# Kernel optimization log

Measured on AMD Instinct MI355X. Metric: run time of the kernel, lower is better.

The kernel has to match this reference:

```python
import jax, jax.numpy as jnp
import numpy as np

N_ATOMS = 100000
N_BONDS = 200000
N_MOLS = 4000
ATOMS_PER_MOL = 25
MAX_NB = 6
ATOM_FDIM = 133
BOND_FDIM = 14
HIDDEN = 300
DEPTH = 3


def setup_inputs() -> dict:
    key = jax.random.key(0)
    ks = jax.random.split(key, 8)
    f_atoms = jax.random.normal(ks[0], (N_ATOMS, ATOM_FDIM), dtype=jnp.float32)
    f_bonds = jax.random.normal(ks[1], (N_BONDS, BOND_FDIM), dtype=jnp.float32)
    # incoming-bond lists per atom (irregular gather targets)
    a2b = jax.random.randint(ks[2], (N_ATOMS, MAX_NB), 0, N_BONDS, dtype=jnp.int32)
    # source atom of each directed bond
    b2a = jax.random.randint(ks[3], (N_BONDS,), 0, N_ATOMS, dtype=jnp.int32)
    # reverse bond: directed bonds come in pairs (2i, 2i+1)
    b2revb = (jnp.arange(N_BONDS, dtype=jnp.int32) ^ 1)
    # contiguous [start, size] per molecule
    starts = jnp.arange(N_MOLS, dtype=jnp.int32) * ATOMS_PER_MOL
    sizes = jnp.full((N_MOLS,), ATOMS_PER_MOL, dtype=jnp.int32)
    a_scope = jnp.stack([starts, sizes], axis=1)
    W_i = jax.random.normal(ks[4], (HIDDEN, ATOM_FDIM + BOND_FDIM), dtype=jnp.float32) * 0.05
    W_h = jax.random.normal(ks[5], (HIDDEN, HIDDEN), dtype=jnp.float32) * 0.05
    W_o = jax.random.normal(ks[6], (HIDDEN, ATOM_FDIM + HIDDEN), dtype=jnp.float32) * 0.05
    b_o = jax.random.normal(ks[7], (HIDDEN,), dtype=jnp.float32) * 0.05
    return {"f_atoms": f_atoms, "f_bonds": f_bonds, "a2b": a2b, "b2a": b2a,
            "b2revb": b2revb, "a_scope": a_scope, "W_i": W_i, "W_h": W_h,
            "W_o": W_o, "b_o": b_o}


def reference(f_atoms, f_bonds, a2b, b2a, b2revb, a_scope, W_i, W_h, W_o, b_o):
    # initial directed-bond messages: [f_atoms[src], f_bonds] -> Linear -> ReLU
    input_feats = jnp.concatenate([f_atoms[b2a], f_bonds], axis=1)  # (E, 147)
    message = jax.nn.relu(input_feats @ W_i.T)  # (E, H)
    for _ in range(DEPTH - 1):
        nei_a_message = message[a2b].sum(axis=1)          # (V, H) gather+sum
        nei_message = nei_a_message[b2a] - message[b2revb]  # (E, H)
        message = jax.nn.relu(nei_message @ W_h.T)
    a_message = message[a2b].sum(axis=1)  # (V, H)
    atom_hiddens = jax.nn.relu(jnp.concatenate([f_atoms, a_message], axis=1) @ W_o.T + b_o)
    # vectorized scope mean-pool (scopes are contiguous ranges)
    starts = a_scope[:, 0]
    sizes = a_scope[:, 1]
    seg_ids = jnp.searchsorted(starts, jnp.arange(atom_hiddens.shape[0]), side='right') - 1
    sums = jax.ops.segment_sum(atom_hiddens, seg_ids, num_segments=N_MOLS)
    denom = jnp.maximum(sizes, 1).astype(atom_hiddens.dtype)[:, None]
    mol_vecs = jnp.where((sizes > 0)[:, None], sums / denom, 0.0)
    return mol_vecs
```

## Files before the change

### kernel.cpp

```cpp
#include <hip/hip_runtime.h>
#include <stdint.h>

#define N_ATOMS   100000
#define N_BONDS   200000
#define N_MOLS    4000
#define MAX_NB    6
#define ATOM_FDIM 133
#define BOND_FDIM 14
#define HIDDEN    300
#define NPAD      320

typedef __attribute__((ext_vector_type(8))) short          bf16x8;
typedef __attribute__((ext_vector_type(8))) unsigned short u16x8;
typedef __attribute__((ext_vector_type(4))) float          f32x4;
typedef __attribute__((ext_vector_type(4))) unsigned int   u32x4;

static __device__ __forceinline__ float u2f(unsigned int u) {
  union { unsigned int u; float f; } v; v.u = u; return v.f;
}
static __device__ __forceinline__ unsigned int f2u(float f) {
  union { float f; unsigned int u; } v; v.f = f; return v.u;
}
static __device__ __forceinline__ float bflo(unsigned int u) { return u2f(u << 16); }
static __device__ __forceinline__ float bfhi(unsigned int u) { return u2f(u & 0xffff0000u); }
static __device__ __forceinline__ unsigned short f2bf_rn(float f) {
  unsigned int u = f2u(f);
  return (unsigned short)((u + 0x7fffu + ((u >> 16) & 1u)) >> 16);
}
static __device__ __forceinline__ unsigned int pack_rn(float lo, float hi) {
  return ((unsigned int)f2bf_rn(hi) << 16) | f2bf_rn(lo);
}

__global__ __launch_bounds__(256) void convin_kernel(
    const float* __restrict__ w, unsigned short* __restrict__ o, int N, int K, int KP) {
  size_t total = (size_t)N * KP;
  for (size_t idx = (size_t)blockIdx.x * 256 + threadIdx.x; idx < total; idx += (size_t)gridDim.x * 256) {
    int n = (int)(idx / KP), k = (int)(idx - (size_t)n * KP);
    float v = (k < K) ? w[(size_t)n * K + k] : 0.f;
    o[idx] = f2bf_rn(v);
  }
}

__global__ __launch_bounds__(256) void convw_kernel(
    const float* __restrict__ w, unsigned short* __restrict__ o,
    int Ksrc, int seg1, int src2off, int seg2dst, int seg2len, int KP) {
  int total = NPAD * KP;
  for (int idx = blockIdx.x * 256 + threadIdx.x; idx < total; idx += gridDim.x * 256) {
    int n = idx / KP, k = idx - n * KP;
    int src = -1;
    if (k < seg1) src = k;
    else if (k >= seg2dst && k < seg2dst + seg2len) src = src2off + (k - seg2dst);
    float v = (n < HIDDEN && src >= 0) ? w[(size_t)n * Ksrc + src] : 0.f;
    o[idx] = f2bf_rn(v);
  }
}

template<int KP, int SEG, bool RELU, bool BIAS>
__global__ __launch_bounds__(256) void gemm_tp(
    const unsigned short* S1, const unsigned short* S2,
    const int* __restrict__ gmap, const unsigned short* __restrict__ W,
    const float* __restrict__ bias, unsigned short* out, int M, int nTiles) {
  constexpr int CHUNKS = KP / 8;
  constexpr int NST    = KP / 32;
  __shared__ __align__(16) unsigned short As[2 * 64 * KP];

  const int tid  = threadIdx.x;
  const int lane = tid & 63;
  const int wv   = tid >> 6;
  const int ar   = lane & 15, kq = lane >> 4;
  const int nbase = wv * 80;
  const unsigned short* Wl = W + (size_t)(nbase + ar) * KP + kq * 8;

  auto rowof = [&](int tile) { int r = tile * 64 + lane; return (r < M) ? r : (M - 1); };

  auto stage = [&](int buf, int drow, int srow) {
    char* base = (char*)As + (size_t)buf * (64 * KP * 2);
#pragma unroll
    for (int cs = wv; cs < CHUNKS; cs += 4) {
      const unsigned short* src;
      if (SEG == 0)      src = S1 + (size_t)drow * KP + cs * 8;
      else if (SEG == 1) src = (cs < 20) ? (S1 + (size_t)srow * 160 + cs * 8)
                                         : (S2 + (size_t)drow * 32 + (cs - 20) * 8);
      else               src = (cs < 20) ? (S1 + (size_t)drow * 160 + cs * 8)
                                         : (S2 + (size_t)drow * NPAD + (cs - 20) * 8);
      __builtin_amdgcn_global_load_lds(
          (const __attribute__((address_space(1))) void*)src,
          (__attribute__((address_space(3))) void*)(base + (size_t)cs * 1024), 16, 0, 0);
    }
  };

  f32x4 acc[4][5];

  auto compute = [&](int buf) {
    const char* base = (const char*)As + (size_t)buf * (64 * KP * 2);
    bf16x8 bnxt[5];
#pragma unroll
    for (int nf = 0; nf < 5; nf++) bnxt[nf] = *(const bf16x8*)(Wl + (size_t)nf * 16 * KP);
#pragma unroll
    for (int ks = 0; ks < NST; ks++) {
      bf16x8 bcur[5];
#pragma unroll
      for (int nf = 0; nf < 5; nf++) bcur[nf] = bnxt[nf];
      if (ks + 1 < NST) {
#pragma unroll
        for (int nf = 0; nf < 5; nf++)
          bnxt[nf] = *(const bf16x8*)(Wl + (size_t)nf * 16 * KP + (ks + 1) * 32);
      }
      bf16x8 af[4];
#pragma unroll
      for (int m = 0; m < 4; m++)
        af[m] = *(const bf16x8*)(base + (size_t)((ks * 4 + kq) * 64 + m * 16 + ar) * 16);
#pragma unroll
      for (int nf = 0; nf < 5; nf++)
#pragma unroll
        for (int m = 0; m < 4; m++)
          acc[m][nf] = __builtin_amdgcn_mfma_f32_16x16x32_bf16(af[m], bcur[nf], acc[m][nf], 0, 0, 0);
    }
  };

  auto storeC = [&](int tile) {
#pragma unroll
    for (int m = 0; m < 4; m++)
#pragma unroll
      for (int rr = 0; rr < 4; rr++) {
        int orow = tile * 64 + m * 16 + kq * 4 + rr;
        if (orow >= M) continue;
#pragma unroll
        for (int nf = 0; nf < 5; nf++) {
          int ocol = nbase + nf * 16 + ar;
          float v = acc[m][nf][rr];
          if (BIAS) v += (ocol < HIDDEN) ? bias[ocol] : 0.f;
          if (RELU) v = v > 0.f ? v : 0.f;
          out[(size_t)orow * NPAD + ocol] = f2bf_rn(v);
        }
      }
  };

  int t = blockIdx.x;
  if (t >= nTiles) return;
  {
    int srow0 = (SEG == 1) ? gmap[rowof(t)] : 0;
    stage(0, rowof(t), srow0);
  }
  int tn = t + gridDim.x;
  int g_n = (SEG == 1 && tn < nTiles) ? gmap[rowof(tn)] : 0;
  __syncthreads();

  int cur = 0;
  while (t < nTiles) {
    const int nxt = t + gridDim.x;
    if (nxt < nTiles) stage(cur ^ 1, rowof(nxt), g_n);
    const int t2 = nxt + gridDim.x;
    int g_n2 = (SEG == 1 && t2 < nTiles) ? gmap[rowof(t2)] : 0;
#pragma unroll
    for (int m = 0; m < 4; m++)
#pragma unroll
      for (int n = 0; n < 5; n++) acc[m][n] = (f32x4){0.f, 0.f, 0.f, 0.f};
    compute(cur);
    __syncthreads();
    storeC(t);
    cur ^= 1; t = nxt; g_n = g_n2;
  }
}

__global__ __launch_bounds__(256) void gemm_tpf(
    const unsigned short* Z, const unsigned short* __restrict__ Nei,
    const int* __restrict__ b2a, const unsigned short* __restrict__ W,
    unsigned short* out, int nTiles) {
  constexpr int KP = 320, NST = 10, NREG = 10;
  __shared__ __align__(16) unsigned short As[2 * 64 * KP];

  const int tid  = threadIdx.x;
  const int lane = tid & 63;
  const int wv   = tid >> 6;
  const int ar   = lane & 15, kq = lane >> 4;
  const int nbase = wv * 80;
  const unsigned short* Wl = W + (size_t)(nbase + ar) * KP + kq * 8;

  u32x4 nei4[NREG], z4[NREG];

  auto loadreg = [&](int tile) {
    const int row = tile * 64 + lane;
    const int g   = b2a[row];
    const int rev = row ^ 1;
#pragma unroll
    for (int i = 0; i < NREG; i++) {
      const int cs = i * 4 + wv;
      nei4[i] = *(const u32x4*)(Nei + (size_t)g * NPAD + cs * 8);
      z4[i]   = *(const u32x4*)(Z + (size_t)rev * NPAD + cs * 8);
    }
  };

  auto writestage = [&](int buf) {
    char* base = (char*)As + (size_t)buf * (64 * KP * 2);
#pragma unroll
    for (int i = 0; i < NREG; i++) {
      const int cs = i * 4 + wv;
      u32x4 o;
#pragma unroll
      for (int t4 = 0; t4 < 4; t4++) {
        float lo = bflo(nei4[i][t4]) - bflo(z4[i][t4]);
        float hi = bfhi(nei4[i][t4]) - bfhi(z4[i][t4]);
        lo = lo > 0.f ? lo : 0.f; hi = hi > 0.f ? hi : 0.f;
        o[t4] = pack_rn(lo, hi);
      }
      *(u32x4*)(base + (size_t)(cs * 64 + lane) * 16) = o;
    }
  };

  f32x4 acc[4][5];

  auto compute = [&](int buf) {
    const char* base = (const char*)As + (size_t)buf * (64 * KP * 2);
    bf16x8 bnxt[5];
#pragma unroll
    for (int nf = 0; nf < 5; nf++) bnxt[nf] = *(const bf16x8*)(Wl + (size_t)nf * 16 * KP);
#pragma unroll
    for (int ks = 0; ks < NST; ks++) {
      bf16x8 bcur[5];
#pragma unroll
      for (int nf = 0; nf < 5; nf++) bcur[nf] = bnxt[nf];
      if (ks + 1 < NST) {
#pragma unroll
        for (int nf = 0; nf < 5; nf++)
          bnxt[nf] = *(const bf16x8*)(Wl + (size_t)nf * 16 * KP + (ks + 1) * 32);
      }
      bf16x8 af[4];
#pragma unroll
      for (int m = 0; m < 4; m++)
        af[m] = *(const bf16x8*)(base + (size_t)((ks * 4 + kq) * 64 + m * 16 + ar) * 16);
#pragma unroll
      for (int nf = 0; nf < 5; nf++)
#pragma unroll
        for (int m = 0; m < 4; m++)
          acc[m][nf] = __builtin_amdgcn_mfma_f32_16x16x32_bf16(af[m], bcur[nf], acc[m][nf], 0, 0, 0);
    }
  };

  auto storeC = [&](int tile) {
#pragma unroll
    for (int m = 0; m < 4; m++)
#pragma unroll
      for (int rr = 0; rr < 4; rr++) {
        int orow = tile * 64 + m * 16 + kq * 4 + rr;
#pragma unroll
        for (int nf = 0; nf < 5; nf++)
          out[(size_t)orow * NPAD + nbase + nf * 16 + ar] =
              f2bf_rn(acc[m][nf][rr]);
      }
  };

  int t = blockIdx.x;
  if (t >= nTiles) return;
  loadreg(t);
  writestage(0);
  __syncthreads();

  int cur = 0;
  while (t < nTiles) {
    const int nxt = t + gridDim.x;
    if (nxt < nTiles) loadreg(nxt);
#pragma unroll
    for (int m = 0; m < 4; m++)
#pragma unroll
      for (int n = 0; n < 5; n++) acc[m][n] = (f32x4){0.f, 0.f, 0.f, 0.f};
    compute(cur);
    if (nxt < nTiles) writestage(cur ^ 1);
    __syncthreads();
    storeC(t);
    cur ^= 1; t = nxt;
  }
}

__global__ __launch_bounds__(256) void agg_kernel(
    const unsigned short* __restrict__ src, const int* __restrict__ a2b,
    unsigned short* __restrict__ dst) {
  const int TPA = NPAD / 16;
  int idx = blockIdx.x * 256 + threadIdx.x;
  if (idx >= N_ATOMS * TPA) return;
  int a  = idx / TPA;
  int kc = (idx - a * TPA) * 16;
  int bidx[MAX_NB];
#pragma unroll
  for (int j = 0; j < MAX_NB; j++) bidx[j] = a2b[a * MAX_NB + j];
  float slo[8], shi[8];
#pragma unroll
  for (int t = 0; t < 8; t++) { slo[t] = 0.f; shi[t] = 0.f; }
#pragma unroll
  for (int j = 0; j < MAX_NB; j++) {
    const u32x4* p = (const u32x4*)(src + (size_t)bidx[j] * NPAD + kc);
    u32x4 v0 = p[0], v1 = p[1];
#pragma unroll
    for (int t = 0; t < 4; t++) {
      slo[t]     += bflo(v0[t]); shi[t]     += bfhi(v0[t]);
      slo[4 + t] += bflo(v1[t]); shi[4 + t] += bfhi(v1[t]);
    }
  }
  u32x4 o0, o1;
#pragma unroll
  for (int t = 0; t < 4; t++) { o0[t] = pack_rn(slo[t], shi[t]); o1[t] = pack_rn(slo[4 + t], shi[4 + t]); }
  u32x4* qp = (u32x4*)(dst + (size_t)a * NPAD + kc);
  qp[0] = o0; qp[1] = o1;
}

__global__ __launch_bounds__(256) void combineH_kernel(
    const unsigned short* __restrict__ neiZ, const unsigned short* Zh,
    const int* __restrict__ b2a, unsigned short* msg) {
  const int TPB = NPAD / 16;
  const int NPAIR = N_BONDS / 2;
  int idx = blockIdx.x * 256 + threadIdx.x;
  if (idx >= NPAIR * TPB) return;
  int p  = idx / TPB;
  int kc = (idx - p * TPB) * 16;
  int b0i = 2 * p, b1i = 2 * p + 1;
  int g0 = b2a[b0i], g1 = b2a[b1i];
  const u32x4* pn0 = (const u32x4*)(neiZ + (size_t)g0 * NPAD + kc);
  const u32x4* pn1 = (const u32x4*)(neiZ + (size_t)g1 * NPAD + kc);
  const u32x4* pz0 = (const u32x4*)(Zh + (size_t)b1i * NPAD + kc);
  const u32x4* pz1 = (const u32x4*)(Zh + (size_t)b0i * NPAD + kc);
  u32x4 n00 = pn0[0], n01 = pn0[1], n10 = pn1[0], n11 = pn1[1];
  u32x4 z00 = pz0[0], z01 = pz0[1], z10 = pz1[0], z11 = pz1[1];
  u32x4 o00, o01, o10, o11;
#pragma unroll
  for (int t = 0; t < 4; t++) {
    float a, c;
    a = bflo(n00[t]) - bflo(z00[t]); c = bfhi(n00[t]) - bfhi(z00[t]);
    o00[t] = pack_rn(a > 0.f ? a : 0.f, c > 0.f ? c : 0.f);
    a = bflo(n01[t]) - bflo(z01[t]); c = bfhi(n01[t]) - bfhi(z01[t]);
    o01[t] = pack_rn(a > 0.f ? a : 0.f, c > 0.f ? c : 0.f);
    a = bflo(n10[t]) - bflo(z10[t]); c = bfhi(n10[t]) - bfhi(z10[t]);
    o10[t] = pack_rn(a > 0.f ? a : 0.f, c > 0.f ? c : 0.f);
    a = bflo(n11[t]) - bflo(z11[t]); c = bfhi(n11[t]) - bfhi(z11[t]);
    o11[t] = pack_rn(a > 0.f ? a : 0.f, c > 0.f ? c : 0.f);
  }
  u32x4* q0 = (u32x4*)(msg + (size_t)b0i * NPAD + kc);
  u32x4* q1 = (u32x4*)(msg + (size_t)b1i * NPAD + kc);
  q0[0] = o00; q0[1] = o01; q1[0] = o10; q1[1] = o11;
}

__global__ __launch_bounds__(256) void readout_kernel(
    const unsigned short* __restrict__ hidden, const int* __restrict__ a_scope,
    float* __restrict__ out) {
  const int TPM = NPAD / 8;
  int idx = blockIdx.x * 256 + threadIdx.x;
  if (idx >= N_MOLS * TPM) return;
  int m = idx / TPM;
  int c = (idx - m * TPM) * 8;
  int start = a_scope[m * 2], size = a_scope[m * 2 + 1];
  float s[8];
#pragma unroll
  for (int t = 0; t < 8; t++) s[t] = 0.f;
  for (int i = 0; i < size; i++) {
    const u32x4 v = *(const u32x4*)(hidden + (size_t)(start + i) * NPAD + c);
#pragma unroll
    for (int t = 0; t < 4; t++) { s[2 * t] += bflo(v[t]); s[2 * t + 1] += bfhi(v[t]); }
  }
  float inv = (size > 0) ? 1.f / (float)size : 0.f;
#pragma unroll
  for (int t = 0; t < 8; t++) {
    int col = c + t;
    if (col < HIDDEN) out[(size_t)m * HIDDEN + col] = s[t] * inv;
  }
}

extern "C" void kernel_launch(void* const* d_in, const int* in_sizes, int n_in,
                              void* d_out, int out_size, void* d_ws, size_t ws_size,
                              hipStream_t stream) {
  const float* f_atoms = (const float*)d_in[0];
  const float* f_bonds = (const float*)d_in[1];
  const int*   a2b     = (const int*)d_in[2];
  const int*   b2a     = (const int*)d_in[3];
  const int*   a_scope = (const int*)d_in[5];
  const float* W_i     = (const float*)d_in[6];
  const float* W_h     = (const float*)d_in[7];
  const float* W_o     = (const float*)d_in[8];
  const float* b_o     = (const float*)d_in[9];
  float* out = (float*)d_out;

  char* ws = (char*)d_ws;
  size_t off = 0;
  auto alloc = [&](size_t bytes) { size_t o = off; off += (bytes + 255) & ~(size_t)255; return o; };
  unsigned short* P     = (unsigned short*)(ws + alloc((size_t)N_BONDS * NPAD * 2));
  unsigned short* R     = (unsigned short*)(ws + alloc((size_t)N_ATOMS * NPAD * 2));
  unsigned short* fa_bf = (unsigned short*)(ws + alloc((size_t)N_ATOMS * 160 * 2));
  unsigned short* fb_bf = (unsigned short*)(ws + alloc((size_t)N_BONDS * 32 * 2));
  unsigned short* WiAB  = (unsigned short*)(ws + alloc((size_t)NPAD * 192 * 2));
  unsigned short* Wh    = (unsigned short*)(ws + alloc((size_t)NPAD * 320 * 2));
  unsigned short* Wo    = (unsigned short*)(ws + alloc((size_t)NPAD * 480 * 2));

  convin_kernel<<<2048, 256, 0, stream>>>(f_atoms, fa_bf, N_ATOMS, ATOM_FDIM, 160);
  convin_kernel<<<2048, 256, 0, stream>>>(f_bonds, fb_bf, N_BONDS, BOND_FDIM, 32);
  convw_kernel<<<(NPAD * 192 + 255) / 256, 256, 0, stream>>>(W_i, WiAB, 147, 133, 133, 160, 14, 192);
  convw_kernel<<<(NPAD * 320 + 255) / 256, 256, 0, stream>>>(W_h, Wh, 300, 300, 0, 0, 0, 320);
  convw_kernel<<<(NPAD * 480 + 255) / 256, 256, 0, stream>>>(W_o, Wo, 433, 133, 133, 160, 300, 480);

  const int nTilesB = N_BONDS / 64;
  const int nTilesA = (N_ATOMS + 63) / 64;
  const int gagg = (N_ATOMS * (NPAD / 16) + 255) / 256;
  const int gpar = ((N_BONDS / 2) * (NPAD / 16) + 255) / 256;

  gemm_tp<192, 1, true, false><<<768, 256, 0, stream>>>(
      fa_bf, fb_bf, b2a, WiAB, nullptr, P, N_BONDS, nTilesB);

  gemm_tp<320, 0, false, false><<<512, 256, 0, stream>>>(
      P, nullptr, nullptr, Wh, nullptr, P, N_BONDS, nTilesB);
  agg_kernel<<<gagg, 256, 0, stream>>>(P, a2b, R);

  gemm_tpf<<<512, 256, 0, stream>>>(P, R, b2a, Wh, P, nTilesB);

  agg_kernel<<<gagg, 256, 0, stream>>>(P, a2b, R);
  combineH_kernel<<<gpar, 256, 0, stream>>>(R, P, b2a, P);

  agg_kernel<<<gagg, 256, 0, stream>>>(P, a2b, R);
  gemm_tp<480, 3, true, true><<<256, 256, 0, stream>>>(
      fa_bf, R, nullptr, Wo, b_o, R, N_ATOMS, nTilesA);

  readout_kernel<<<(N_MOLS * (NPAD / 8) + 255) / 256, 256, 0, stream>>>(R, a_scope, out);
}
```

Measured before the change: 658.8 us.

## Split GEMM K dimension into double-buffered chunks to shrink LDS footprint

The tiled GEMM now stages each 64-row A tile in K-chunks (two for the input and hidden GEMMs, three for the output GEMM) instead of the whole K width. It double-buffers across chunks and tiles, cutting shared-memory use per block so more blocks can be resident per CU, and grid sizes are raised to match. The trade-off is more barriers per tile. The gather-map prefetch for the next tile is also dropped, so the index load now sits on the staging path.

After: 695.4 us. 5.6% more time.

```diff
diff --git a/kernel.cpp b/kernel.cpp
--- a/kernel.cpp
+++ b/kernel.cpp
@@ -55,14 +55,15 @@
   }
 }
 
-template<int KP, int SEG, bool RELU, bool BIAS>
-__global__ __launch_bounds__(256) void gemm_tp(
+template<int KP, int NCH, int SEG, bool RELU, bool BIAS>
+__global__ __launch_bounds__(256) void gemm_tpc(
     const unsigned short* S1, const unsigned short* S2,
     const int* __restrict__ gmap, const unsigned short* __restrict__ W,
     const float* __restrict__ bias, unsigned short* out, int M, int nTiles) {
-  constexpr int CHUNKS = KP / 8;
-  constexpr int NST    = KP / 32;
-  __shared__ __align__(16) unsigned short As[2 * 64 * KP];
+  constexpr int BK   = KP / NCH;
+  constexpr int NSTC = BK / 32;
+  constexpr int CHG  = BK / 8;
+  __shared__ __align__(16) unsigned short As[2 * 64 * BK];
 
   const int tid  = threadIdx.x;
   const int lane = tid & 63;
@@ -71,40 +72,44 @@
   const int nbase = wv * 80;
   const unsigned short* Wl = W + (size_t)(nbase + ar) * KP + kq * 8;
 
-  auto rowof = [&](int tile) { int r = tile * 64 + lane; return (r < M) ? r : (M - 1); };
-
-  auto stage = [&](int buf, int drow, int srow) {
-    char* base = (char*)As + (size_t)buf * (64 * KP * 2);
-#pragma unroll
-    for (int cs = wv; cs < CHUNKS; cs += 4) {
+  auto stage = [&](int buf, int tile, int chunk) {
+    char* base = (char*)As + (size_t)buf * (64 * BK * 2);
+    int r = tile * 64 + lane; if (r >= M) r = M - 1;
+    int srow = 0;
+    if (SEG == 1) srow = gmap[r];
+#pragma unroll
+    for (int cl = wv; cl < CHG; cl += 4) {
+      const int cs = chunk * CHG + cl;
+      const int ae = cs * 8;
       const unsigned short* src;
-      if (SEG == 0)      src = S1 + (size_t)drow * KP + cs * 8;
-      else if (SEG == 1) src = (cs < 20) ? (S1 + (size_t)srow * 160 + cs * 8)
-                                         : (S2 + (size_t)drow * 32 + (cs - 20) * 8);
-      else               src = (cs < 20) ? (S1 + (size_t)drow * 160 + cs * 8)
-                                         : (S2 + (size_t)drow * NPAD + (cs - 20) * 8);
+      if (SEG == 0)      src = S1 + (size_t)r * KP + ae;
+      else if (SEG == 1) src = (cs < 20) ? (S1 + (size_t)srow * 160 + ae)
+                                         : (S2 + (size_t)r * 32 + (ae - 160));
+      else               src = (cs < 20) ? (S1 + (size_t)r * 160 + ae)
+                                         : (S2 + (size_t)r * NPAD + (ae - 160));
       __builtin_amdgcn_global_load_lds(
           (const __attribute__((address_space(1))) void*)src,
-          (__attribute__((address_space(3))) void*)(base + (size_t)cs * 1024), 16, 0, 0);
+          (__attribute__((address_space(3))) void*)(base + (size_t)cl * 1024), 16, 0, 0);
     }
   };
 
   f32x4 acc[4][5];
 
-  auto compute = [&](int buf) {
-    const char* base = (const char*)As + (size_t)buf * (64 * KP * 2);
+  auto compute = [&](int buf, int chunk) {
+    const char* base = (const char*)As + (size_t)buf * (64 * BK * 2);
+    const int kb = chunk * BK;
     bf16x8 bnxt[5];
 #pragma unroll
-    for (int nf = 0; nf < 5; nf++) bnxt[nf] = *(const bf16x8*)(Wl + (size_t)nf * 16 * KP);
-#pragma unroll
-    for (int ks = 0; ks < NST; ks++) {
+    for (int nf = 0; nf < 5; nf++) bnxt[nf] = *(const bf16x8*)(Wl + (size_t)nf * 16 * KP + kb);
+#pragma unroll
+    for (int ks = 0; ks < NSTC; ks++) {
       bf16x8 bcur[5];
 #pragma unroll
       for (int nf = 0; nf < 5; nf++) bcur[nf] = bnxt[nf];
-      if (ks + 1 < NST) {
+      if (ks + 1 < NSTC) {
 #pragma unroll
         for (int nf = 0; nf < 5; nf++)
-          bnxt[nf] = *(const bf16x8*)(Wl + (size_t)nf * 16 * KP + (ks + 1) * 32);
+          bnxt[nf] = *(const bf16x8*)(Wl + (size_t)nf * 16 * KP + kb + (ks + 1) * 32);
       }
       bf16x8 af[4];
 #pragma unroll
@@ -138,28 +143,26 @@
 
   int t = blockIdx.x;
   if (t >= nTiles) return;
-  {
-    int srow0 = (SEG == 1) ? gmap[rowof(t)] : 0;
-    stage(0, rowof(t), srow0);
-  }
-  int tn = t + gridDim.x;
-  int g_n = (SEG == 1 && tn < nTiles) ? gmap[rowof(tn)] : 0;
+  stage(0, t, 0);
   __syncthreads();
 
   int cur = 0;
   while (t < nTiles) {
-    const int nxt = t + gridDim.x;
-    if (nxt < nTiles) stage(cur ^ 1, rowof(nxt), g_n);
-    const int t2 = nxt + gridDim.x;
-    int g_n2 = (SEG == 1 && t2 < nTiles) ? gmap[rowof(t2)] : 0;
 #pragma unroll
     for (int m = 0; m < 4; m++)
 #pragma unroll
       for (int n = 0; n < 5; n++) acc[m][n] = (f32x4){0.f, 0.f, 0.f, 0.f};
-    compute(cur);
-    __syncthreads();
+#pragma unroll
+    for (int c = 0; c < NCH; c++) {
+      int nt = t, nc = c + 1;
+      if (nc == NCH) { nt = t + gridDim.x; nc = 0; }
+      if (nt < nTiles) stage(cur ^ 1, nt, nc);
+      compute(cur, c);
+      __syncthreads();
+      cur ^= 1;
+    }
     storeC(t);
-    cur ^= 1; t = nxt; g_n = g_n2;
+    t += gridDim.x;
   }
 }
 
@@ -245,8 +248,7 @@
         int orow = tile * 64 + m * 16 + kq * 4 + rr;
 #pragma unroll
         for (int nf = 0; nf < 5; nf++)
-          out[(size_t)orow * NPAD + nbase + nf * 16 + ar] =
-              f2bf_rn(acc[m][nf][rr]);
+          out[(size_t)orow * NPAD + nbase + nf * 16 + ar] = f2bf_rn(acc[m][nf][rr]);
       }
   };
 
@@ -399,10 +401,10 @@
   const int gagg = (N_ATOMS * (NPAD / 16) + 255) / 256;
   const int gpar = ((N_BONDS / 2) * (NPAD / 16) + 255) / 256;
 
-  gemm_tp<192, 1, true, false><<<768, 256, 0, stream>>>(
+  gemm_tpc<192, 2, 1, true, false><<<1024, 256, 0, stream>>>(
       fa_bf, fb_bf, b2a, WiAB, nullptr, P, N_BONDS, nTilesB);
 
-  gemm_tp<320, 0, false, false><<<512, 256, 0, stream>>>(
+  gemm_tpc<320, 2, 0, false, false><<<1024, 256, 0, stream>>>(
       P, nullptr, nullptr, Wh, nullptr, P, N_BONDS, nTilesB);
   agg_kernel<<<gagg, 256, 0, stream>>>(P, a2b, R);
 
@@ -412,7 +414,7 @@
   combineH_kernel<<<gpar, 256, 0, stream>>>(R, P, b2a, P);
 
   agg_kernel<<<gagg, 256, 0, stream>>>(P, a2b, R);
-  gemm_tp<480, 3, true, true><<<256, 256, 0, stream>>>(
+  gemm_tpc<480, 3, 3, true, true><<<784, 256, 0, stream>>>(
       fa_bf, R, nullptr, Wo, b_o, R, N_ATOMS, nTilesA);
 
   readout_kernel<<<(N_MOLS * (NPAD / 8) + 255) / 256, 256, 0, stream>>>(R, a_scope, out);
```
